# Performance work log

Measured on AMD Instinct MI355X. Metric: run time of the kernel, lower is better.

Reference implementation:

```python
import jax, jax.numpy as jnp
import numpy as np


def setup_inputs() -> dict:
    key = jax.random.key(0)
    k1, k2, k3 = jax.random.split(key, 3)
    shape = (8, 2, 1024, 1024)
    predict = jax.random.normal(k1, shape, dtype=jnp.float32)
    target = jax.random.normal(k2, shape, dtype=jnp.float32)
    weight = jax.random.uniform(k3, shape, dtype=jnp.float32)
    return {"predict": predict, "target": target, "weight": weight, "min_kept": 2000000}


def reference(predict, target, weight, min_kept):
    # norm_term = prod(spatial dims) * batch  (channels NOT included, per source)
    B = predict.shape[0]
    spatial = float(np.prod(predict.shape[2:]))
    norm_term = jnp.float32(spatial * B)

    sq = (predict - target) ** 2
    loss_flat = (sq / norm_term).reshape(-1)          # unweighted per-elem MSE
    # threshold = sorted_ascending[N - min_kept] == min_kept-th largest value.
    # top_k replaces the full sort (same order statistic, ties identical).
    topk_vals, _ = jax.lax.top_k(loss_flat, min_kept)
    threshold = topk_vals[min_kept - 1]

    wloss_flat = (weight * sq / norm_term).reshape(-1)
    mask = loss_flat > threshold                      # strict >, as in source
    cnt = jnp.sum(mask)
    # reduction == 'elementwise_mean': mean over selected elements
    return jnp.sum(jnp.where(mask, wloss_flat, 0.0)) / cnt.astype(wloss_flat.dtype)
```

## Files before the change

### kernel.cpp

```cpp
#include <hip/hip_runtime.h>
#include <stdint.h>


#define H2_BITS 17
#define H1_SIZE 32768
#define H2_SIZE 131072
#define SHARDS 64

#define OFF_H2   131072
#define OFF_META 655360
#define OFF_SUMS 655424
#define OFF_SHC  655488
#define OFF_CAND 786432

__global__ __launch_bounds__(256) void k_zero(uint32_t* ws, int n) {
    int i = blockIdx.x * 256 + threadIdx.x;
    if (i < n) ws[i] = 0;
}

__global__ __launch_bounds__(1024) void k_hist1(
    const float4* __restrict__ p, const float4* __restrict__ t,
    uint32_t* __restrict__ hist1, int n4)
{
    __shared__ uint32_t lh[H1_SIZE / 2];
    for (int i = threadIdx.x; i < H1_SIZE / 2; i += 1024) lh[i] = 0;
    __syncthreads();
    const int stride = gridDim.x * 1024;
    for (int i = blockIdx.x * 1024 + threadIdx.x; i < n4; i += stride) {
        float4 pv = p[i], tv = t[i];
        float d0 = pv.x - tv.x, d1 = pv.y - tv.y, d2 = pv.z - tv.z, d3 = pv.w - tv.w;
        uint32_t b0 = __float_as_uint(d0 * d0 * 0x1p-23f) >> H2_BITS;
        uint32_t b1 = __float_as_uint(d1 * d1 * 0x1p-23f) >> H2_BITS;
        uint32_t b2 = __float_as_uint(d2 * d2 * 0x1p-23f) >> H2_BITS;
        uint32_t b3 = __float_as_uint(d3 * d3 * 0x1p-23f) >> H2_BITS;
        atomicAdd(&lh[b0 >> 1], 1u << ((b0 & 1) * 16));
        atomicAdd(&lh[b1 >> 1], 1u << ((b1 & 1) * 16));
        atomicAdd(&lh[b2 >> 1], 1u << ((b2 & 1) * 16));
        atomicAdd(&lh[b3 >> 1], 1u << ((b3 & 1) * 16));
    }
    __syncthreads();
    for (int i = threadIdx.x; i < H1_SIZE / 2; i += 1024) {
        uint32_t v = lh[i];
        uint32_t c0 = v & 0xFFFFu, c1 = v >> 16;
        if (c0) atomicAdd(&hist1[2 * i], c0);
        if (c1) atomicAdd(&hist1[2 * i + 1], c1);
    }
}

__global__ __launch_bounds__(1024) void k_scan1(
    const uint32_t* __restrict__ hist1, const int* __restrict__ min_kept,
    uint32_t* __restrict__ meta)
{
    __shared__ uint32_t psum[1024];
    __shared__ uint32_t gsuf[64];
    const int t = threadIdx.x;
    const uint32_t k = (uint32_t)(*min_kept);
    const int per = H1_SIZE / 1024;
    const int base = t * per;
    uint32_t s = 0;
    #pragma unroll
    for (int i = 0; i < per; i++) s += hist1[base + i];
    psum[t] = s;
    __syncthreads();
    if (t < 64) {
        uint32_t g = 0;
        for (int i = 0; i < 16; i++) g += psum[t * 16 + i];
        uint32_t v = g;
        #pragma unroll
        for (int off = 1; off < 64; off <<= 1) {
            uint32_t o = __shfl_down(v, off);
            if (t + off < 64) v += o;
        }
        gsuf[t] = v;
    }
    __syncthreads();
    const int g = t >> 4;
    uint32_t cum = (g < 63) ? gsuf[g + 1] : 0;
    const int gend = g * 16 + 15;
    for (int j = t + 1; j <= gend; j++) cum += psum[j];
    if (cum < k && k <= cum + psum[t]) {
        uint32_t c = cum;
        for (int i = per - 1; i >= 0; i--) {
            uint32_t h = hist1[base + i];
            c += h;
            if (c >= k) {
                meta[0] = (uint32_t)(base + i);
                meta[1] = k - (c - h);
                break;
            }
        }
    }
}

__global__ __launch_bounds__(256) void k_main(
    const float4* __restrict__ p, const float4* __restrict__ t,
    const float4* __restrict__ w,
    uint32_t* meta, uint32_t* __restrict__ hist2,
    double* __restrict__ sums, uint32_t* __restrict__ shard_cnt,
    uint2* __restrict__ cand, uint32_t cap_per_shard, int n4)
{
    const uint32_t b = meta[0];
    double lsum = 0.0;
    uint32_t lcnt = 0;
    const int shard = blockIdx.x & (SHARDS - 1);
    uint32_t* my_cnt = &shard_cnt[shard];
    uint2* my_cand = cand + (size_t)shard * cap_per_shard;
    const int stride = gridDim.x * 256;
    for (int i = blockIdx.x * 256 + threadIdx.x; i < n4; i += stride) {
        float4 pv = p[i], tv = t[i], wv = w[i];
        float pd[4] = {pv.x - tv.x, pv.y - tv.y, pv.z - tv.z, pv.w - tv.w};
        float wa[4] = {wv.x, wv.y, wv.z, wv.w};
        #pragma unroll
        for (int c = 0; c < 4; c++) {
            float loss = pd[c] * pd[c] * 0x1p-23f;
            uint32_t bits = __float_as_uint(loss);
            uint32_t hi = bits >> H2_BITS;
            if (hi > b) {
                lcnt++;
                lsum += (double)(wa[c] * loss);
            } else if (hi == b) {
                atomicAdd(&hist2[bits & (H2_SIZE - 1)], 1u);
                uint32_t idx = atomicAdd(my_cnt, 1u);
                if (idx < cap_per_shard) {
                    my_cand[idx] = make_uint2(bits, __float_as_uint(wa[c]));
                } else {
                    meta[3] = 1u;
                }
            }
        }
    }
    #pragma unroll
    for (int off = 32; off; off >>= 1) {
        lsum += __shfl_down(lsum, off);
        lcnt += __shfl_down(lcnt, off);
    }
    __shared__ double sred[4];
    __shared__ uint32_t cred[4];
    const int wid = threadIdx.x >> 6, lane = threadIdx.x & 63;
    if (lane == 0) { sred[wid] = lsum; cred[wid] = lcnt; }
    __syncthreads();
    if (threadIdx.x == 0) {
        double bs = sred[0] + sred[1] + sred[2] + sred[3];
        uint32_t bc = cred[0] + cred[1] + cred[2] + cred[3];
        atomicAdd(&sums[0], bs);
        atomicAdd(&meta[4], bc);
    }
}

__global__ __launch_bounds__(1024) void k_scan2(
    const uint32_t* __restrict__ hist2, uint32_t* meta)
{
    __shared__ uint32_t psum[1024];
    __shared__ uint32_t gsuf[64];
    const int t = threadIdx.x;
    const uint32_t k = meta[1];
    const uint32_t b = meta[0];
    const int per = H2_SIZE / 1024;
    const int base = t * per;
    uint32_t s = 0;
    for (int i = 0; i < per; i++) s += hist2[base + i];
    psum[t] = s;
    __syncthreads();
    if (t < 64) {
        uint32_t g = 0;
        for (int i = 0; i < 16; i++) g += psum[t * 16 + i];
        uint32_t v = g;
        #pragma unroll
        for (int off = 1; off < 64; off <<= 1) {
            uint32_t o = __shfl_down(v, off);
            if (t + off < 64) v += o;
        }
        gsuf[t] = v;
    }
    __syncthreads();
    const int g = t >> 4;
    uint32_t cum = (g < 63) ? gsuf[g + 1] : 0;
    const int gend = g * 16 + 15;
    for (int j = t + 1; j <= gend; j++) cum += psum[j];
    if (cum < k && k <= cum + psum[t]) {
        uint32_t c = cum;
        for (int i = per - 1; i >= 0; i--) {
            uint32_t h = hist2[base + i];
            c += h;
            if (c >= k) {
                meta[2] = (b << H2_BITS) | (uint32_t)(base + i);
                break;
            }
        }
    }
}

__global__ __launch_bounds__(256) void k_cand(
    const float4* __restrict__ p, const float4* __restrict__ t,
    const float4* __restrict__ w,
    uint32_t* meta, const uint32_t* __restrict__ shard_cnt,
    const uint2* __restrict__ cand, uint32_t cap_per_shard,
    double* __restrict__ sums, int n4)
{
    const uint32_t thr = meta[2];
    const uint32_t overflow = meta[3];
    double lsum = 0.0;
    uint32_t lcnt = 0;
    if (!overflow) {
        for (int sdx = 0; sdx < SHARDS; sdx++) {
            uint32_t cnt = shard_cnt[sdx];
            if (cnt > cap_per_shard) cnt = cap_per_shard;
            const uint2* cs = cand + (size_t)sdx * cap_per_shard;
            for (uint32_t i = blockIdx.x * 256 + threadIdx.x; i < cnt;
                 i += gridDim.x * 256) {
                uint2 e = cs[i];
                if (e.x > thr) {
                    lcnt++;
                    lsum += (double)(__uint_as_float(e.y) * __uint_as_float(e.x));
                }
            }
        }
    } else {
        const uint32_t b = meta[0];
        const int stride = gridDim.x * 256;
        for (int i = blockIdx.x * 256 + threadIdx.x; i < n4; i += stride) {
            float4 pv = p[i], tv = t[i], wv = w[i];
            float pd[4] = {pv.x - tv.x, pv.y - tv.y, pv.z - tv.z, pv.w - tv.w};
            float wa[4] = {wv.x, wv.y, wv.z, wv.w};
            #pragma unroll
            for (int c = 0; c < 4; c++) {
                float loss = pd[c] * pd[c] * 0x1p-23f;
                uint32_t bits = __float_as_uint(loss);
                if ((bits >> H2_BITS) == b && bits > thr) {
                    lcnt++;
                    lsum += (double)(wa[c] * loss);
                }
            }
        }
    }
    #pragma unroll
    for (int off = 32; off; off >>= 1) {
        lsum += __shfl_down(lsum, off);
        lcnt += __shfl_down(lcnt, off);
    }
    __shared__ double sred[4];
    __shared__ uint32_t cred[4];
    const int wid = threadIdx.x >> 6, lane = threadIdx.x & 63;
    if (lane == 0) { sred[wid] = lsum; cred[wid] = lcnt; }
    __syncthreads();
    if (threadIdx.x == 0) {
        double bs = sred[0] + sred[1] + sred[2] + sred[3];
        uint32_t bc = cred[0] + cred[1] + cred[2] + cred[3];
        atomicAdd(&sums[1], bs);
        atomicAdd(&meta[5], bc);
    }
}

__global__ __launch_bounds__(64) void k_final(
    const double* __restrict__ sums, const uint32_t* __restrict__ meta,
    float* __restrict__ out)
{
    if (threadIdx.x == 0 && blockIdx.x == 0) {
        double s = sums[0] + sums[1];
        double c = (double)(meta[4] + meta[5]);
        out[0] = (float)(s / c);
    }
}

extern "C" void kernel_launch(void* const* d_in, const int* in_sizes, int n_in,
                              void* d_out, int out_size, void* d_ws, size_t ws_size,
                              hipStream_t stream) {
    const float* p = (const float*)d_in[0];
    const float* t = (const float*)d_in[1];
    const float* w = (const float*)d_in[2];
    const int* mk = (const int*)d_in[3];
    float* out = (float*)d_out;
    const int n = in_sizes[0];
    const int n4 = n / 4;

    uint8_t* ws = (uint8_t*)d_ws;
    uint32_t* hist1 = (uint32_t*)ws;
    uint32_t* hist2 = (uint32_t*)(ws + OFF_H2);
    uint32_t* meta  = (uint32_t*)(ws + OFF_META);
    double*   sums  = (double*)(ws + OFF_SUMS);
    uint32_t* shcnt = (uint32_t*)(ws + OFF_SHC);
    uint2*    cand  = (uint2*)(ws + OFF_CAND);
    uint32_t cap_per_shard = 0;
    if (ws_size > OFF_CAND + SHARDS * 8) {
        cap_per_shard = (uint32_t)((ws_size - OFF_CAND) / (8 * SHARDS));
    }

    k_zero<<<(OFF_CAND / 4 + 255) / 256, 256, 0, stream>>>((uint32_t*)ws, OFF_CAND / 4);
    k_hist1<<<512, 1024, 0, stream>>>((const float4*)p, (const float4*)t, hist1, n4);
    k_scan1<<<1, 1024, 0, stream>>>(hist1, mk, meta);
    k_main<<<2048, 256, 0, stream>>>((const float4*)p, (const float4*)t,
                                     (const float4*)w, meta, hist2, sums, shcnt,
                                     cand, cap_per_shard, n4);
    k_scan2<<<1, 1024, 0, stream>>>(hist2, meta);
    k_cand<<<2048, 256, 0, stream>>>((const float4*)p, (const float4*)t,
                                     (const float4*)w, meta, shcnt, cand,
                                     cap_per_shard, sums, n4);
    k_final<<<1, 64, 0, stream>>>(sums, meta, out);
}
```

Before: 404.4 us.

## Unroll loads, aggregate candidate atomics per wave, split global histogram, shrink cand grid

The histogram kernel now unrolls four strided float4 loads per iteration, writes into two global histogram copies chosen by block parity, and rotates its flush order to spread atomic contention. The main pass unrolls by two and replaces the per-element candidate-counter atomic with one wave-aggregated atomic built from ballot and popcount. Zeroing uses hipMemsetAsync instead of a custom kernel, and the candidate kernel launches fewer blocks. These target atomic contention and memory latency, at the cost of a larger workspace layout and extra per-element ballot work in the main loop.

```diff
diff --git a/kernel.cpp b/kernel.cpp
--- a/kernel.cpp
+++ b/kernel.cpp
@@ -4,46 +4,57 @@
 
 #define H2_BITS 17
 #define H1_SIZE 32768
+#define H1_WORDS (H1_SIZE / 2)
 #define H2_SIZE 131072
 #define SHARDS 64
 
-#define OFF_H2   131072
-#define OFF_META 655360
-#define OFF_SUMS 655424
-#define OFF_SHC  655488
-#define OFF_CAND 786432
-
-__global__ __launch_bounds__(256) void k_zero(uint32_t* ws, int n) {
-    int i = blockIdx.x * 256 + threadIdx.x;
-    if (i < n) ws[i] = 0;
+#define OFF_H2   262144
+#define OFF_META 786432
+#define OFF_SUMS 786496
+#define OFF_SHC  786560
+#define OFF_CAND 786944
+
+__device__ __forceinline__ void hist_add4(uint32_t* lh, float4 pv, float4 tv) {
+    float d0 = pv.x - tv.x, d1 = pv.y - tv.y, d2 = pv.z - tv.z, d3 = pv.w - tv.w;
+    uint32_t b0 = __float_as_uint(d0 * d0 * 0x1p-23f) >> H2_BITS;
+    uint32_t b1 = __float_as_uint(d1 * d1 * 0x1p-23f) >> H2_BITS;
+    uint32_t b2 = __float_as_uint(d2 * d2 * 0x1p-23f) >> H2_BITS;
+    uint32_t b3 = __float_as_uint(d3 * d3 * 0x1p-23f) >> H2_BITS;
+    atomicAdd(&lh[b0 >> 1], 1u << ((b0 & 1) * 16));
+    atomicAdd(&lh[b1 >> 1], 1u << ((b1 & 1) * 16));
+    atomicAdd(&lh[b2 >> 1], 1u << ((b2 & 1) * 16));
+    atomicAdd(&lh[b3 >> 1], 1u << ((b3 & 1) * 16));
 }
 
 __global__ __launch_bounds__(1024) void k_hist1(
     const float4* __restrict__ p, const float4* __restrict__ t,
     uint32_t* __restrict__ hist1, int n4)
 {
-    __shared__ uint32_t lh[H1_SIZE / 2];
-    for (int i = threadIdx.x; i < H1_SIZE / 2; i += 1024) lh[i] = 0;
-    __syncthreads();
-    const int stride = gridDim.x * 1024;
-    for (int i = blockIdx.x * 1024 + threadIdx.x; i < n4; i += stride) {
-        float4 pv = p[i], tv = t[i];
-        float d0 = pv.x - tv.x, d1 = pv.y - tv.y, d2 = pv.z - tv.z, d3 = pv.w - tv.w;
-        uint32_t b0 = __float_as_uint(d0 * d0 * 0x1p-23f) >> H2_BITS;
-        uint32_t b1 = __float_as_uint(d1 * d1 * 0x1p-23f) >> H2_BITS;
-        uint32_t b2 = __float_as_uint(d2 * d2 * 0x1p-23f) >> H2_BITS;
-        uint32_t b3 = __float_as_uint(d3 * d3 * 0x1p-23f) >> H2_BITS;
-        atomicAdd(&lh[b0 >> 1], 1u << ((b0 & 1) * 16));
-        atomicAdd(&lh[b1 >> 1], 1u << ((b1 & 1) * 16));
-        atomicAdd(&lh[b2 >> 1], 1u << ((b2 & 1) * 16));
-        atomicAdd(&lh[b3 >> 1], 1u << ((b3 & 1) * 16));
-    }
-    __syncthreads();
-    for (int i = threadIdx.x; i < H1_SIZE / 2; i += 1024) {
-        uint32_t v = lh[i];
+    __shared__ uint32_t lh[H1_WORDS];
+    for (int j = threadIdx.x; j < H1_WORDS; j += 1024) lh[j] = 0;
+    __syncthreads();
+    const int S = gridDim.x * 1024;
+    int i = blockIdx.x * 1024 + threadIdx.x;
+    for (; i + 3 * S < n4; i += 4 * S) {
+        float4 pv0 = p[i],         tv0 = t[i];
+        float4 pv1 = p[i + S],     tv1 = t[i + S];
+        float4 pv2 = p[i + 2 * S], tv2 = t[i + 2 * S];
+        float4 pv3 = p[i + 3 * S], tv3 = t[i + 3 * S];
+        hist_add4(lh, pv0, tv0);
+        hist_add4(lh, pv1, tv1);
+        hist_add4(lh, pv2, tv2);
+        hist_add4(lh, pv3, tv3);
+    }
+    for (; i < n4; i += S) hist_add4(lh, p[i], t[i]);
+    __syncthreads();
+    uint32_t* dst = hist1 + (blockIdx.x & 1) * H1_SIZE;
+    const uint32_t rot = (blockIdx.x >> 1) * 64;
+    for (int jj = threadIdx.x; jj < H1_WORDS; jj += 1024) {
+        int j = (int)((jj + rot) & (H1_WORDS - 1));
+        uint32_t v = lh[j];
         uint32_t c0 = v & 0xFFFFu, c1 = v >> 16;
-        if (c0) atomicAdd(&hist1[2 * i], c0);
-        if (c1) atomicAdd(&hist1[2 * i + 1], c1);
+        if (c0) atomicAdd(&dst[2 * j], c0);
+        if (c1) atomicAdd(&dst[2 * j + 1], c1);
     }
 }
 
@@ -55,11 +66,13 @@
     __shared__ uint32_t gsuf[64];
     const int t = threadIdx.x;
     const uint32_t k = (uint32_t)(*min_kept);
+    const uint32_t* h0 = hist1;
+    const uint32_t* h1 = hist1 + H1_SIZE;
     const int per = H1_SIZE / 1024;
     const int base = t * per;
     uint32_t s = 0;
     #pragma unroll
-    for (int i = 0; i < per; i++) s += hist1[base + i];
+    for (int i = 0; i < per; i++) s += h0[base + i] + h1[base + i];
     psum[t] = s;
     __syncthreads();
     if (t < 64) {
@@ -81,7 +94,7 @@
     if (cum < k && k <= cum + psum[t]) {
         uint32_t c = cum;
         for (int i = per - 1; i >= 0; i--) {
-            uint32_t h = hist1[base + i];
+            uint32_t h = h0[base + i] + h1[base + i];
             c += h;
             if (c >= k) {
                 meta[0] = (uint32_t)(base + i);
@@ -105,30 +118,50 @@
     const int shard = blockIdx.x & (SHARDS - 1);
     uint32_t* my_cnt = &shard_cnt[shard];
     uint2* my_cand = cand + (size_t)shard * cap_per_shard;
-    const int stride = gridDim.x * 256;
-    for (int i = blockIdx.x * 256 + threadIdx.x; i < n4; i += stride) {
-        float4 pv = p[i], tv = t[i], wv = w[i];
-        float pd[4] = {pv.x - tv.x, pv.y - tv.y, pv.z - tv.z, pv.w - tv.w};
+    const int lane = threadIdx.x & 63;
+
+    auto proc = [&](float4 pv, float4 tv, float4 wv) {
+        float d[4] = {pv.x - tv.x, pv.y - tv.y, pv.z - tv.z, pv.w - tv.w};
         float wa[4] = {wv.x, wv.y, wv.z, wv.w};
         #pragma unroll
         for (int c = 0; c < 4; c++) {
-            float loss = pd[c] * pd[c] * 0x1p-23f;
+            float loss = d[c] * d[c] * 0x1p-23f;
             uint32_t bits = __float_as_uint(loss);
             uint32_t hi = bits >> H2_BITS;
             if (hi > b) {
                 lcnt++;
                 lsum += (double)(wa[c] * loss);
-            } else if (hi == b) {
-                atomicAdd(&hist2[bits & (H2_SIZE - 1)], 1u);
-                uint32_t idx = atomicAdd(my_cnt, 1u);
-                if (idx < cap_per_shard) {
-                    my_cand[idx] = make_uint2(bits, __float_as_uint(wa[c]));
-                } else {
-                    meta[3] = 1u;
+            }
+            unsigned long long m = __ballot(hi == b);
+            if (m) {
+                if (hi == b) {
+                    int pos = __popcll(m & ((1ull << lane) - 1ull));
+                    int leader = __ffsll(m) - 1;
+                    uint32_t base_ = 0;
+                    if (lane == leader)
+                        base_ = atomicAdd(my_cnt, (uint32_t)__popcll(m));
+                    base_ = __shfl(base_, leader);
+                    uint32_t idx = base_ + (uint32_t)pos;
+                    if (idx < cap_per_shard)
+                        my_cand[idx] = make_uint2(bits, __float_as_uint(wa[c]));
+                    else
+                        meta[3] = 1u;
+                    atomicAdd(&hist2[bits & (H2_SIZE - 1)], 1u);
                 }
             }
         }
-    }
+    };
+
+    const int S = gridDim.x * 256;
+    int i = blockIdx.x * 256 + threadIdx.x;
+    for (; i + S < n4; i += 2 * S) {
+        float4 pv0 = p[i],     tv0 = t[i],     wv0 = w[i];
+        float4 pv1 = p[i + S], tv1 = t[i + S], wv1 = w[i + S];
+        proc(pv0, tv0, wv0);
+        proc(pv1, tv1, wv1);
+    }
+    for (; i < n4; i += S) proc(p[i], t[i], w[i]);
+
     #pragma unroll
     for (int off = 32; off; off >>= 1) {
         lsum += __shfl_down(lsum, off);
@@ -136,7 +169,7 @@
     }
     __shared__ double sred[4];
     __shared__ uint32_t cred[4];
-    const int wid = threadIdx.x >> 6, lane = threadIdx.x & 63;
+    const int wid = threadIdx.x >> 6;
     if (lane == 0) { sred[wid] = lsum; cred[wid] = lcnt; }
     __syncthreads();
     if (threadIdx.x == 0) {
@@ -216,17 +249,17 @@
             }
         }
     } else {
-        const uint32_t b = meta[0];
-        const int stride = gridDim.x * 256;
-        for (int i = blockIdx.x * 256 + threadIdx.x; i < n4; i += stride) {
+        const uint32_t bb = meta[0];
+        const int S = gridDim.x * 256;
+        for (int i = blockIdx.x * 256 + threadIdx.x; i < n4; i += S) {
             float4 pv = p[i], tv = t[i], wv = w[i];
-            float pd[4] = {pv.x - tv.x, pv.y - tv.y, pv.z - tv.z, pv.w - tv.w};
+            float d[4] = {pv.x - tv.x, pv.y - tv.y, pv.z - tv.z, pv.w - tv.w};
             float wa[4] = {wv.x, wv.y, wv.z, wv.w};
             #pragma unroll
             for (int c = 0; c < 4; c++) {
-                float loss = pd[c] * pd[c] * 0x1p-23f;
+                float loss = d[c] * d[c] * 0x1p-23f;
                 uint32_t bits = __float_as_uint(loss);
-                if ((bits >> H2_BITS) == b && bits > thr) {
+                if ((bits >> H2_BITS) == bb && bits > thr) {
                     lcnt++;
                     lsum += (double)(wa[c] * loss);
                 }
@@ -285,15 +318,15 @@
         cap_per_shard = (uint32_t)((ws_size - OFF_CAND) / (8 * SHARDS));
     }
 
-    k_zero<<<(OFF_CAND / 4 + 255) / 256, 256, 0, stream>>>((uint32_t*)ws, OFF_CAND / 4);
+    hipMemsetAsync(d_ws, 0, OFF_CAND, stream);
     k_hist1<<<512, 1024, 0, stream>>>((const float4*)p, (const float4*)t, hist1, n4);
     k_scan1<<<1, 1024, 0, stream>>>(hist1, mk, meta);
     k_main<<<2048, 256, 0, stream>>>((const float4*)p, (const float4*)t,
                                      (const float4*)w, meta, hist2, sums, shcnt,
                                      cand, cap_per_shard, n4);
     k_scan2<<<1, 1024, 0, stream>>>(hist2, meta);
-    k_cand<<<2048, 256, 0, stream>>>((const float4*)p, (const float4*)t,
-                                     (const float4*)w, meta, shcnt, cand,
-                                     cap_per_shard, sums, n4);
+    k_cand<<<256, 256, 0, stream>>>((const float4*)p, (const float4*)t,
+                                    (const float4*)w, meta, shcnt, cand,
+                                    cap_per_shard, sums, n4);
     k_final<<<1, 64, 0, stream>>>(sums, meta, out);
 }
```

Result: faster. 386.1 us (-4.5%).
